# Performance work log

Measured on AMD Instinct MI355X. Metric: run time of the kernel, lower is better.

## Reference

```python
import jax, jax.numpy as jnp
import numpy as np

B, S, D, H, L = 64, 512, 1024, 1024, 2


def setup_inputs() -> dict:
    key = jax.random.key(0)
    ks = jax.random.split(key, 12)
    x = jax.random.normal(ks[0], (B, S, D), dtype=jnp.float32)
    lengths = jax.random.randint(ks[1], (B,), 1, S + 1)
    lengths = lengths.at[0].set(S)  # ensure max len == S (matches torch trim)
    x_mask = (jnp.arange(S)[None, :] < lengths[:, None]).astype(jnp.float32)
    h0 = jax.random.normal(ks[2], (L, B, H), dtype=jnp.float32)
    sc = 1.0 / np.sqrt(H)
    p = {}
    p['Wih0'] = jax.random.uniform(ks[3], (3 * H, D), jnp.float32, -sc, sc)
    p['Whh0'] = jax.random.uniform(ks[4], (3 * H, H), jnp.float32, -sc, sc)
    p['bih0'] = jax.random.uniform(ks[5], (3 * H,), jnp.float32, -sc, sc)
    p['bhh0'] = jax.random.uniform(ks[6], (3 * H,), jnp.float32, -sc, sc)
    p['Wih1'] = jax.random.uniform(ks[7], (3 * H, H), jnp.float32, -sc, sc)
    p['Whh1'] = jax.random.uniform(ks[8], (3 * H, H), jnp.float32, -sc, sc)
    p['bih1'] = jax.random.uniform(ks[9], (3 * H,), jnp.float32, -sc, sc)
    p['bhh1'] = jax.random.uniform(ks[10], (3 * H,), jnp.float32, -sc, sc)
    return dict(x=x, x_mask=x_mask, h0=h0, **p)


def _gru_cell(xt, h, Wih, Whh, bih, bhh):
    # PyTorch gate order: r, z, n
    gi = xt @ Wih.T + bih          # [B, 3H]
    gh = h @ Whh.T + bhh           # [B, 3H]
    ir, iz, inn = jnp.split(gi, 3, axis=-1)
    hr, hz, hn = jnp.split(gh, 3, axis=-1)
    r = jax.nn.sigmoid(ir + hr)
    z = jax.nn.sigmoid(iz + hz)
    n = jnp.tanh(inn + r * hn)
    return (1.0 - z) * n + z * h


def reference(x, x_mask, h0, Wih0, Whh0, bih0, bhh0, Wih1, Whh1, bih1, bhh1):
    params = [(Wih0, Whh0, bih0, bhh0), (Wih1, Whh1, bih1, bhh1)]
    xs = jnp.swapaxes(x, 0, 1)        # [S, B, D]
    ms = x_mask.T                     # [S, B]

    def step(h, inp):
        xt, mt = inp                  # [B, D], [B]
        gate = (mt > 0.5)[:, None]    # packed seq: skip padded steps
        layer_in = xt
        new_hs = []
        for l, (Wih, Whh, bih, bhh) in enumerate(params):
            hl = h[l]
            hl_new = jnp.where(gate, _gru_cell(layer_in, hl, Wih, Whh, bih, bhh), hl)
            new_hs.append(hl_new)
            layer_in = hl_new
        h_new = jnp.stack(new_hs)
        return h_new, new_hs[-1] * mt[:, None]  # masked top-layer output

    h_final, outs = jax.lax.scan(step, h0, (xs, ms))
    output_pad = jnp.swapaxes(outs, 0, 1)        # [B, S, H]
    hidden = jnp.swapaxes(h_final, 0, 1)         # [B, L, H]
    return jnp.concatenate([output_pad, hidden], axis=1).mean(axis=1, keepdims=True)
```

## Files before the change

### kernel.cpp

```cpp
#include <hip/hip_runtime.h>
#include <hip/hip_fp16.h>

#define BB 64
#define SS 512
#define DD 1024
#define HH 1024
#define TICKS 515
#define NBLK 128

typedef _Float16 f16;
typedef unsigned long long u64;
typedef __attribute__((ext_vector_type(8))) _Float16 f16x8;
typedef __attribute__((ext_vector_type(4))) _Float16 f16x4;
typedef __attribute__((ext_vector_type(4))) float f32x4;

struct GruWS {
  unsigned cnt[4 * 8 * 64];
  f16 gi0[4][3 * HH][BB];
  f16 gi1[4][3 * HH][BB];
  f16 h0b[4][BB][HH];
  f16 h1b[4][BB][HH];
};

__device__ __forceinline__ f16x8 ld_sys_16B(const void* p) {
  f16x8 r;
  asm volatile("global_load_dwordx4 %0, %1, off sc0 sc1" : "=v"(r) : "v"(p) : "memory");
  return r;
}
__device__ __forceinline__ void st_sys_16B(void* p, f16x8 v) {
  asm volatile("global_store_dwordx4 %0, %1, off sc0 sc1" :: "v"(p), "v"(v) : "memory");
}
__device__ __forceinline__ void drain_vm() {
  asm volatile("s_waitcnt vmcnt(0)" ::: "memory");
  __builtin_amdgcn_sched_barrier(0);
}
__device__ __forceinline__ f16x4 ld_sys_f16x4(const f16* p) {
  u64 q = __hip_atomic_load((const u64*)p, __ATOMIC_RELAXED, __HIP_MEMORY_SCOPE_SYSTEM);
  union { u64 q; f16x4 v; } u; u.q = q; return u.v;
}
__device__ __forceinline__ float ld_sys_f16s(const f16* p) {
  unsigned short s = __hip_atomic_load((const unsigned short*)p, __ATOMIC_RELAXED, __HIP_MEMORY_SCOPE_SYSTEM);
  union { unsigned short s; f16 h; } u; u.s = s; return (float)u.h;
}
__device__ __forceinline__ void st_sys_u16(f16* p, f16 v) {
  union { f16 h; unsigned short s; } u; u.h = v;
  __hip_atomic_store((unsigned short*)p, u.s, __ATOMIC_RELAXED, __HIP_MEMORY_SCOPE_SYSTEM);
}

__device__ __forceinline__ void wait_done(unsigned* cnt, int role, int tick) {
  if (tick < 0) return;
  unsigned* c = &cnt[(role * 8 + (tick & 7)) * 64];
  const unsigned tgt = 32u * ((unsigned)tick / 8u + 1u);
  while (__hip_atomic_load(c, __ATOMIC_RELAXED, __HIP_MEMORY_SCOPE_SYSTEM) < tgt)
    __builtin_amdgcn_s_sleep(4);
  asm volatile("" ::: "memory");
}

__global__ void gru_init(const float* __restrict__ h0, GruWS* __restrict__ ws) {
  int i = blockIdx.x * 256 + threadIdx.x;
  if (i < BB * HH) {
    st_sys_u16(&ws->h0b[3][0][i], (f16)h0[i]);
  } else if (i < 2 * BB * HH) {
    st_sys_u16(&ws->h1b[3][0][i - BB * HH], (f16)h0[i]);
  }
  if (i < 4 * 8) {
    __hip_atomic_store(&ws->cnt[i * 64], 0u, __ATOMIC_RELAXED, __HIP_MEMORY_SCOPE_SYSTEM);
  }
}

__device__ __forceinline__ void mma_pass(const f16x8 areg[8][4], const f16x8* bnt,
                                         float* red, int lane, int wave, f32x4 acc[3]) {
  f32x4 pacc[4][3];
#pragma unroll
  for (int m = 0; m < 4; ++m)
#pragma unroll
    for (int g = 0; g < 3; ++g) pacc[m][g] = (f32x4){0.f, 0.f, 0.f, 0.f};
#pragma unroll
  for (int kk = 0; kk < 8; ++kk)
#pragma unroll
    for (int m = 0; m < 4; ++m)
#pragma unroll
      for (int g = 0; g < 3; ++g)
        pacc[m][g] = __builtin_amdgcn_mfma_f32_16x16x32_f16(areg[kk][m], bnt[g * 8 + kk], pacc[m][g], 0, 0, 0);
#pragma unroll
  for (int m = 0; m < 4; ++m)
    if (m != wave)
#pragma unroll
      for (int g = 0; g < 3; ++g)
#pragma unroll
        for (int r = 0; r < 4; ++r)
          red[(((wave * 4 + m) * 3 + g) * 4 + r) * 64 + lane] = pacc[m][g][r];
  __syncthreads();
#pragma unroll
  for (int g = 0; g < 3; ++g) {
    f32x4 a = pacc[wave][g];
#pragma unroll
    for (int sw = 0; sw < 4; ++sw)
      if (sw != wave)
#pragma unroll
        for (int r = 0; r < 4; ++r)
          a[r] += red[(((sw * 4 + wave) * 3 + g) * 4 + r) * 64 + lane];
    acc[g] = a;
  }
}

__global__ __launch_bounds__(256, 1) void gru_main(
    const float* __restrict__ x, const float* __restrict__ xmask,
    const float* __restrict__ h0in,
    const float* __restrict__ Wih0, const float* __restrict__ Whh0,
    const float* __restrict__ bih0, const float* __restrict__ bhh0,
    const float* __restrict__ Wih1, const float* __restrict__ Whh1,
    const float* __restrict__ bih1, const float* __restrict__ bhh1,
    float* __restrict__ out, GruWS* __restrict__ ws) {
  __shared__ __align__(16) char ldsbuf[49152];
  float* red = (float*)ldsbuf;

  const int bid = blockIdx.x;
  const int grp = bid >> 5;
  const int gidx = bid & 31;
  const int base = gidx * 32;
  const int tid = threadIdx.x;
  const int lane = tid & 63;
  const int wave = tid >> 6;
  const int l15 = lane & 15;
  const int kgrp = lane >> 4;
  const int b0 = wave * 16 + kgrp * 4;
  const int kbase0 = wave * 256 + kgrp * 8;
  unsigned* cnt = ws->cnt;

  const float* Wsrc = (grp == 0) ? Wih0 : (grp == 1) ? Whh0 : (grp == 2) ? Wih1 : Whh1;
  f16x8 breg[2][3][8];
#pragma unroll
  for (int nt = 0; nt < 2; ++nt)
#pragma unroll
    for (int g = 0; g < 3; ++g)
#pragma unroll
      for (int kk = 0; kk < 8; ++kk) {
        const float* p = Wsrc + (long)(g * HH + base + nt * 16 + l15) * DD + kbase0 + kk * 32;
        float4 v0 = *(const float4*)p;
        float4 v1 = *(const float4*)(p + 4);
        f16x8 t;
        t[0] = (f16)v0.x; t[1] = (f16)v0.y; t[2] = (f16)v0.z; t[3] = (f16)v0.w;
        t[4] = (f16)v1.x; t[5] = (f16)v1.y; t[6] = (f16)v1.z; t[7] = (f16)v1.w;
        breg[nt][g][kk] = t;
      }

  if (grp == 0 || grp == 2) {
    const int layer = (grp == 2);
    const float* bih = layer ? bih1 : bih0;
    const float* bhh = layer ? bhh1 : bhh0;
    float bias[2][3];
#pragma unroll
    for (int nt = 0; nt < 2; ++nt)
#pragma unroll
      for (int g = 0; g < 3; ++g) {
        int colg = base + nt * 16 + l15;
        bias[nt][g] = bih[g * HH + colg] + (g < 2 ? bhh[g * HH + colg] : 0.0f);
      }

    for (int t = 0; t < TICKS; ++t) {
      const int s = t - (layer ? 2 : 0);
      const bool active = (s >= 0 && s < SS);
      if (tid == 0 && active) {
        if (!layer) {
          wait_done(cnt, 1, t - 3);
        } else {
          wait_done(cnt, 1, t - 1);
          wait_done(cnt, 3, t - 3);
        }
      }
      __syncthreads();
      if (active) {
        f16x8 areg[8][4];
        if (!layer) {
#pragma unroll
          for (int kk = 0; kk < 8; ++kk)
#pragma unroll
            for (int m = 0; m < 4; ++m) {
              const float* p = x + (long)(m * 16 + l15) * (SS * DD) + (long)s * DD + kbase0 + kk * 32;
              float4 v0 = *(const float4*)p;
              float4 v1 = *(const float4*)(p + 4);
              f16x8 a;
              a[0] = (f16)v0.x; a[1] = (f16)v0.y; a[2] = (f16)v0.z; a[3] = (f16)v0.w;
              a[4] = (f16)v1.x; a[5] = (f16)v1.y; a[6] = (f16)v1.z; a[7] = (f16)v1.w;
              areg[kk][m] = a;
            }
        } else {
          const f16* A = &ws->h0b[s & 3][0][0];
#pragma unroll
          for (int kk = 0; kk < 8; ++kk)
#pragma unroll
            for (int m = 0; m < 4; ++m)
              areg[kk][m] = ld_sys_16B(A + (long)(m * 16 + l15) * HH + kbase0 + kk * 32);
          drain_vm();
        }
        f32x4 accs[2][3];
        mma_pass(areg, &breg[0][0][0], red, lane, wave, accs[0]);
        __syncthreads();
        mma_pass(areg, &breg[1][0][0], red, lane, wave, accs[1]);
        __syncthreads();

        f16* gt = (f16*)ldsbuf;
#pragma unroll
        for (int nt = 0; nt < 2; ++nt)
#pragma unroll
          for (int g = 0; g < 3; ++g) {
            f16x4 o;
#pragma unroll
            for (int r = 0; r < 4; ++r) o[r] = (f16)(accs[nt][g][r] + bias[nt][g]);
            *(f16x4*)(gt + (g * 32 + nt * 16 + l15) * 64 + b0) = o;
          }
        __syncthreads();
        f16* gib = layer ? &ws->gi1[s & 3][0][0] : &ws->gi0[s & 3][0][0];
#pragma unroll
        for (int rnd = 0; rnd < 3; ++rnd) {
          int idx = rnd * 256 + tid;
          int row = idx >> 3, ch = idx & 7;
          int g = row >> 5, c = row & 31;
          f16x8 v = *(const f16x8*)(gt + row * 64 + ch * 8);
          st_sys_16B(gib + (long)(g * HH + base + c) * BB + ch * 8, v);
        }
      }
      asm volatile("s_waitcnt vmcnt(0)" ::: "memory");
      __syncthreads();
      if (tid == 0)
        __hip_atomic_fetch_add(&cnt[(grp * 8 + (t & 7)) * 64], 1u,
                               __ATOMIC_RELAXED, __HIP_MEMORY_SCOPE_SYSTEM);
    }
  } else {
    const int layer = (grp == 3);
    const float* bhh = layer ? bhh1 : bhh0;
    float bhn[2], hold[2][4], osum[2][4];
#pragma unroll
    for (int nt = 0; nt < 2; ++nt) {
      bhn[nt] = bhh[2 * HH + base + nt * 16 + l15];
#pragma unroll
      for (int r = 0; r < 4; ++r) {
        hold[nt][r] = h0in[(long)layer * BB * HH + (long)(b0 + r) * HH + base + nt * 16 + l15];
        osum[nt][r] = 0.f;
      }
    }

    for (int t = 0; t < TICKS; ++t) {
      const int s = t - (layer ? 3 : 1);
      const bool active = (s >= 0 && s < SS);
      if (tid == 0 && active) {
        if (!layer) {
          wait_done(cnt, 0, t - 1);
          wait_done(cnt, 1, t - 1);
          wait_done(cnt, 2, t - 3);
        } else {
          wait_done(cnt, 2, t - 1);
          wait_done(cnt, 3, t - 1);
        }
      }
      __syncthreads();
      if (active) {
        const f16* hprev = layer ? &ws->h1b[(s - 1) & 3][0][0] : &ws->h0b[(s - 1) & 3][0][0];
        const f16* gib = layer ? &ws->gi1[s & 3][0][0] : &ws->gi0[s & 3][0][0];
        f16x8 areg[8][4];
#pragma unroll
        for (int kk = 0; kk < 8; ++kk)
#pragma unroll
          for (int m = 0; m < 4; ++m)
            areg[kk][m] = ld_sys_16B(hprev + (long)(m * 16 + l15) * HH + kbase0 + kk * 32);
        f16x4 gfr[2][3];
#pragma unroll
        for (int nt = 0; nt < 2; ++nt)
#pragma unroll
          for (int g = 0; g < 3; ++g)
            gfr[nt][g] = ld_sys_f16x4(gib + (long)(g * HH + base + nt * 16 + l15) * BB + b0);
        float mv[4];
#pragma unroll
        for (int r = 0; r < 4; ++r) mv[r] = xmask[(long)(b0 + r) * SS + s];
        drain_vm();

        f32x4 accs[2][3];
        mma_pass(areg, &breg[0][0][0], red, lane, wave, accs[0]);
        __syncthreads();
        mma_pass(areg, &breg[1][0][0], red, lane, wave, accs[1]);
        __syncthreads();

        f16* htile = (f16*)ldsbuf;
#pragma unroll
        for (int nt = 0; nt < 2; ++nt)
#pragma unroll
          for (int r = 0; r < 4; ++r) {
            float pr = accs[nt][0][r] + (float)gfr[nt][0][r];
            float pz = accs[nt][1][r] + (float)gfr[nt][1][r];
            float ph = accs[nt][2][r] + bhn[nt];
            float rr = 1.0f / (1.0f + __expf(-pr));
            float zz = 1.0f / (1.0f + __expf(-pz));
            float nn = tanhf((float)gfr[nt][2][r] + rr * ph);
            float upd = hold[nt][r] + (1.0f - zz) * (nn - hold[nt][r]);
            if (mv[r] > 0.5f) {
              hold[nt][r] = upd;
              if (layer) osum[nt][r] += upd;
            }
            htile[(b0 + r) * 32 + nt * 16 + l15] = (f16)hold[nt][r];
          }
        __syncthreads();
        f16* hout = layer ? &ws->h1b[s & 3][0][0] : &ws->h0b[s & 3][0][0];
        {
          int b = tid >> 2, ch = tid & 3;
          f16x8 v = *(const f16x8*)(htile + b * 32 + ch * 8);
          st_sys_16B(hout + (long)b * HH + base + ch * 8, v);
        }
        if (s == SS - 1 && layer) {
#pragma unroll
          for (int nt = 0; nt < 2; ++nt)
#pragma unroll
            for (int r = 0; r < 4; ++r) {
              int colg = base + nt * 16 + l15;
              float h0f = ld_sys_f16s(&ws->h0b[3][b0 + r][colg]);
              out[(long)(b0 + r) * HH + colg] =
                  (osum[nt][r] + hold[nt][r] + h0f) * (1.0f / 514.0f);
            }
        }
      }
      asm volatile("s_waitcnt vmcnt(0)" ::: "memory");
      __syncthreads();
      if (tid == 0)
        __hip_atomic_fetch_add(&cnt[(grp * 8 + (t & 7)) * 64], 1u,
                               __ATOMIC_RELAXED, __HIP_MEMORY_SCOPE_SYSTEM);
    }
  }
}

extern "C" void kernel_launch(void* const* d_in, const int* in_sizes, int n_in,
                              void* d_out, int out_size, void* d_ws, size_t ws_size,
                              hipStream_t stream) {
  const float* x = (const float*)d_in[0];
  const float* xmask = (const float*)d_in[1];
  const float* h0 = (const float*)d_in[2];
  const float* Wih0 = (const float*)d_in[3];
  const float* Whh0 = (const float*)d_in[4];
  const float* bih0 = (const float*)d_in[5];
  const float* bhh0 = (const float*)d_in[6];
  const float* Wih1 = (const float*)d_in[7];
  const float* Whh1 = (const float*)d_in[8];
  const float* bih1 = (const float*)d_in[9];
  const float* bhh1 = (const float*)d_in[10];
  float* out = (float*)d_out;
  GruWS* ws = (GruWS*)d_ws;

  hipLaunchKernelGGL(gru_init, dim3((2 * BB * HH) / 256), dim3(256), 0, stream, h0, ws);
  hipLaunchKernelGGL(gru_main, dim3(NBLK), dim3(256), 0, stream,
                     x, xmask, h0, Wih0, Whh0, bih0, bhh0,
                     Wih1, Whh1, bih1, bhh1, out, ws);
}
```

Baseline: 9.967 ms.

## Use sc1 atomic swaps for cross-block stores and parallelize dependency waits

Cross-block stores of gate inputs and hidden state are changed from sc0 sc1 dwordx4 stores to pairs of 64-bit atomic swaps with sc1 only. The intent is to keep the data at a cache level shared across blocks (the helper is named for MALL) and shorten the store-to-load path between producer and consumer blocks. Dependency waits on several counters are spread across separate threads so they poll in parallel, and the spin sleep interval is shortened. The init kernel is vectorized to four elements per thread with fewer blocks. Atomic swaps may cost more issue slots than plain stores, and the coherence guarantee now relies on atomics being performed at the shared cache level.

```diff
diff --git a/kernel.cpp b/kernel.cpp
--- a/kernel.cpp
+++ b/kernel.cpp
@@ -27,8 +27,13 @@
   asm volatile("global_load_dwordx4 %0, %1, off sc0 sc1" : "=v"(r) : "v"(p) : "memory");
   return r;
 }
-__device__ __forceinline__ void st_sys_16B(void* p, f16x8 v) {
-  asm volatile("global_store_dwordx4 %0, %1, off sc0 sc1" :: "v"(p), "v"(v) : "memory");
+__device__ __forceinline__ void st_mall_16B(void* p, f16x8 v) {
+  union { f16x8 v; u64 q[2]; } u; u.v = v;
+  asm volatile("global_atomic_swap_x2 %0, %1, off sc1" :: "v"((u64*)p), "v"(u.q[0]) : "memory");
+  asm volatile("global_atomic_swap_x2 %0, %1, off sc1" :: "v"((u64*)p + 1), "v"(u.q[1]) : "memory");
+}
+__device__ __forceinline__ void st_mall_8B(void* p, u64 q) {
+  asm volatile("global_atomic_swap_x2 %0, %1, off sc1" :: "v"((u64*)p), "v"(q) : "memory");
 }
 __device__ __forceinline__ void drain_vm() {
   asm volatile("s_waitcnt vmcnt(0)" ::: "memory");
@@ -41,10 +46,6 @@
 __device__ __forceinline__ float ld_sys_f16s(const f16* p) {
   unsigned short s = __hip_atomic_load((const unsigned short*)p, __ATOMIC_RELAXED, __HIP_MEMORY_SCOPE_SYSTEM);
   union { unsigned short s; f16 h; } u; u.s = s; return (float)u.h;
-}
-__device__ __forceinline__ void st_sys_u16(f16* p, f16 v) {
-  union { f16 h; unsigned short s; } u; u.h = v;
-  __hip_atomic_store((unsigned short*)p, u.s, __ATOMIC_RELAXED, __HIP_MEMORY_SCOPE_SYSTEM);
 }
 
 __device__ __forceinline__ void wait_done(unsigned* cnt, int role, int tick) {
@@ -52,16 +53,19 @@
   unsigned* c = &cnt[(role * 8 + (tick & 7)) * 64];
   const unsigned tgt = 32u * ((unsigned)tick / 8u + 1u);
   while (__hip_atomic_load(c, __ATOMIC_RELAXED, __HIP_MEMORY_SCOPE_SYSTEM) < tgt)
-    __builtin_amdgcn_s_sleep(4);
+    __builtin_amdgcn_s_sleep(2);
   asm volatile("" ::: "memory");
 }
 
 __global__ void gru_init(const float* __restrict__ h0, GruWS* __restrict__ ws) {
   int i = blockIdx.x * 256 + threadIdx.x;
-  if (i < BB * HH) {
-    st_sys_u16(&ws->h0b[3][0][i], (f16)h0[i]);
-  } else if (i < 2 * BB * HH) {
-    st_sys_u16(&ws->h1b[3][0][i - BB * HH], (f16)h0[i]);
+  int j = i * 4;
+  if (j < 2 * BB * HH) {
+    union { f16 h[4]; u64 q; } u;
+#pragma unroll
+    for (int k = 0; k < 4; ++k) u.h[k] = (f16)h0[j + k];
+    if (j < BB * HH) st_mall_8B(&ws->h0b[3][0][j], u.q);
+    else             st_mall_8B(&ws->h1b[3][0][j - BB * HH], u.q);
   }
   if (i < 4 * 8) {
     __hip_atomic_store(&ws->cnt[i * 64], 0u, __ATOMIC_RELAXED, __HIP_MEMORY_SCOPE_SYSTEM);
@@ -161,13 +165,12 @@
     for (int t = 0; t < TICKS; ++t) {
       const int s = t - (layer ? 2 : 0);
       const bool active = (s >= 0 && s < SS);
-      if (tid == 0 && active) {
-        if (!layer) {
-          wait_done(cnt, 1, t - 3);
-        } else {
-          wait_done(cnt, 1, t - 1);
-          wait_done(cnt, 3, t - 3);
-        }
+      if (active && tid < 2) {
+        int role, tk;
+        if (!layer) { role = 1; tk = (tid == 0) ? t - 3 : -1; }
+        else        { role = (tid == 0) ? 1 : 3;
+                      tk   = (tid == 0) ? t - 1 : t - 3; }
+        wait_done(cnt, role, tk);
       }
       __syncthreads();
       if (active) {
@@ -218,7 +221,7 @@
           int row = idx >> 3, ch = idx & 7;
           int g = row >> 5, c = row & 31;
           f16x8 v = *(const f16x8*)(gt + row * 64 + ch * 8);
-          st_sys_16B(gib + (long)(g * HH + base + c) * BB + ch * 8, v);
+          st_mall_16B(gib + (long)(g * HH + base + c) * BB + ch * 8, v);
         }
       }
       asm volatile("s_waitcnt vmcnt(0)" ::: "memory");
@@ -244,15 +247,16 @@
     for (int t = 0; t < TICKS; ++t) {
       const int s = t - (layer ? 3 : 1);
       const bool active = (s >= 0 && s < SS);
-      if (tid == 0 && active) {
+      if (active && tid < 3) {
+        int role, tk;
         if (!layer) {
-          wait_done(cnt, 0, t - 1);
-          wait_done(cnt, 1, t - 1);
-          wait_done(cnt, 2, t - 3);
+          role = (tid == 0) ? 0 : (tid == 1) ? 1 : 2;
+          tk   = (tid == 2) ? t - 3 : t - 1;
         } else {
-          wait_done(cnt, 2, t - 1);
-          wait_done(cnt, 3, t - 1);
-        }
+          role = (tid == 0) ? 2 : 3;
+          tk   = (tid < 2) ? t - 1 : -1;
+        }
+        wait_done(cnt, role, tk);
       }
       __syncthreads();
       if (active) {
@@ -304,7 +308,7 @@
         {
           int b = tid >> 2, ch = tid & 3;
           f16x8 v = *(const f16x8*)(htile + b * 32 + ch * 8);
-          st_sys_16B(hout + (long)b * HH + base + ch * 8, v);
+          st_mall_16B(hout + (long)b * HH + base + ch * 8, v);
         }
         if (s == SS - 1 && layer) {
 #pragma unroll
@@ -344,7 +348,7 @@
   float* out = (float*)d_out;
   GruWS* ws = (GruWS*)d_ws;
 
-  hipLaunchKernelGGL(gru_init, dim3((2 * BB * HH) / 256), dim3(256), 0, stream, h0, ws);
+  hipLaunchKernelGGL(gru_init, dim3(128), dim3(256), 0, stream, h0, ws);
   hipLaunchKernelGGL(gru_main, dim3(NBLK), dim3(256), 0, stream,
                      x, xmask, h0, Wih0, Whh0, bih0, bhh0,
                      Wih1, Whh1, bih1, bhh1, out, ws);
```

New measurement: 10.10 ms. Within noise of the previous version (+1.4%).
